# Kernel tuning notes

Measured on AMD Instinct MI355X. Metric: run time of the kernel, lower is better.

The kernel has to match this reference:

```python
import jax, jax.numpy as jnp
import numpy as np

N = 100000      # nodes (single ntype 'paper' for the reference)
R = 4           # relations
E = 300000      # edges per relation
P = 2           # prediction relations (pred_in_n_rev_etypes)
FEAT = 64       # feat_len
H = 64          # gen_h_dim
B = 2           # num_bases
NUM_PRED = 5
S = 4096        # seed nodes


def setup_inputs() -> dict:
    key = jax.random.key(0)
    ks = jax.random.split(key, 26)
    sc = 0.05
    inp = {
        "x": jax.random.normal(ks[0], (N, FEAT), jnp.float32),
        "edges": jax.random.randint(ks[1], (R, E, 2), 0, N, dtype=jnp.int32),
        "seeds": jax.random.randint(ks[2], (S,), 0, N, dtype=jnp.int32),
        "noise": jax.random.normal(ks[3], (N, H), jnp.float32),
        # RelGraphConv layer 1 (basis decomposition) and layer 2
        "V1": jax.random.normal(ks[4], (B, FEAT, H), jnp.float32) * sc,
        "C1": jax.random.normal(ks[5], (R, B), jnp.float32) * sc,
        "V2": jax.random.normal(ks[6], (B, H, H), jnp.float32) * sc,
        "C2": jax.random.normal(ks[7], (R, B), jnp.float32) * sc,
        # per-ntype linear head
        "W_lin": jax.random.normal(ks[8], (H, H), jnp.float32) * sc,
        "b_lin": jnp.zeros((H,), jnp.float32),
        # ReldGen per-relation MLP: H->256->32->1
        "Wd1": jax.random.normal(ks[9], (P, H, 256), jnp.float32) * sc,
        "bd1": jnp.zeros((P, 256), jnp.float32),
        "Wd2": jax.random.normal(ks[10], (P, 256, 32), jnp.float32) * sc,
        "bd2": jnp.zeros((P, 32), jnp.float32),
        "Wd3": jax.random.normal(ks[11], (P, 32, 1), jnp.float32) * sc,
        "bd3": jnp.zeros((P, 1), jnp.float32),
        # RelfGen per-relation MLP: H->256->2048->NUM_PRED*FEAT
        "Wf1": jax.random.normal(ks[12], (P, H, 256), jnp.float32) * sc,
        "bf1": jnp.zeros((P, 256), jnp.float32),
        "Wf2": jax.random.normal(ks[13], (P, 256, 2048), jnp.float32) * sc,
        "bf2": jnp.zeros((P, 2048), jnp.float32),
        "Wf3": jax.random.normal(ks[14], (P, 2048, NUM_PRED * FEAT), jnp.float32) * sc,
        "bf3": jnp.zeros((P, NUM_PRED * FEAT), jnp.float32),
    }
    return inp


def _rel_conv(h, V, C, edges):
    # basis decomposition: W_r = sum_b C[r,b] * V[b]
    Wr = jnp.einsum('rb,bio->rio', C, V)          # [R, in, out]
    m = jnp.einsum('ni,rio->rno', h, Wr)           # transform-then-gather

    def per_rel(m_r, e_r):
        msg = m_r[e_r[:, 0]]                       # gather src  [E, out]
        agg = jax.ops.segment_sum(msg, e_r[:, 1], num_segments=N)
        deg = jax.ops.segment_sum(jnp.ones((e_r.shape[0],), m_r.dtype),
                                  e_r[:, 1], num_segments=N)
        return agg / jnp.maximum(deg, 1.0)[:, None]  # GraphConv norm='right'

    out = jax.vmap(per_rel)(m, edges)              # [R, N, out]
    return jax.nn.relu(out.sum(axis=0))            # HeteroGraphConv 'sum' + relu


def reference(x, edges, seeds, noise, V1, C1, V2, C2, W_lin, b_lin,
              Wd1, bd1, Wd2, bd2, Wd3, bd3, Wf1, bf1, Wf2, bf2, Wf3, bf3):
    h = _rel_conv(x, V1, C1, edges)                # layer 1: FEAT -> H
    h = _rel_conv(h, V2, C2, edges)                # layer 2: H -> H
    h = jax.nn.leaky_relu(h @ W_lin + b_lin)       # per-ntype linear head
    h = h + noise                                  # Sampler: h + N(0,1)
    hs = h[seeds]                                  # [S, H]
    # ReldGen: predicted missing-neighbor counts per relation
    d = jax.nn.leaky_relu(jnp.einsum('sh,phk->psk', hs, Wd1) + bd1[:, None, :])
    d = jax.nn.leaky_relu(jnp.einsum('psk,pkm->psm', d, Wd2) + bd2[:, None, :])
    pred_missing = jax.nn.relu(jnp.einsum('psm,pmo->pso', d, Wd3) + bd3[:, None, :])  # [P,S,1]
    # RelfGen: predicted neighbor features per relation
    f = jax.nn.relu(jnp.einsum('sh,phk->psk', hs, Wf1) + bf1[:, None, :])
    f = jax.nn.relu(jnp.einsum('psk,pkm->psm', f, Wf2) + bf2[:, None, :])
    f = jnp.tanh(jnp.einsum('psm,pmo->pso', f, Wf3) + bf3[:, None, :])
    pred_feat = f.reshape(P, S, NUM_PRED, FEAT)
    return pred_missing, pred_feat
```

## Files before the change

kernel.cpp:

```cpp
#include <hip/hip_runtime.h>
#include <math.h>

#define NN 100000
#define RR 4
#define EE 300000
#define PP 2
#define HH 64
#define SS 4096
#define NSEG (NN * RR)
#define FPART 8
#define PWIDTH ((NN + FPART - 1) / FPART)

typedef __attribute__((ext_vector_type(8))) short short8;
typedef __attribute__((ext_vector_type(4))) short short4v;
typedef __attribute__((ext_vector_type(4))) float f32x4;
typedef __attribute__((ext_vector_type(2))) unsigned int u32x2;

__device__ __forceinline__ short f2bf(float v) {
    unsigned u = __float_as_uint(v);
    unsigned r = (u + 0x7FFFu + ((u >> 16) & 1u)) >> 16;
    return (short)r;
}
__device__ __forceinline__ float bf2f(short s) {
    return __uint_as_float(((unsigned)(unsigned short)s) << 16);
}
__device__ __forceinline__ float bflo(unsigned v) { return __uint_as_float(v << 16); }
__device__ __forceinline__ float bfhi(unsigned v) { return __uint_as_float(v & 0xFFFF0000u); }
__device__ __forceinline__ unsigned pack2(float a, float b) {
    return (unsigned)(unsigned short)f2bf(a) | ((unsigned)(unsigned short)f2bf(b) << 16);
}

struct PrepPtrs {
    const float *Wlin, *Wd1, *Wd2, *Wf1, *Wf2, *Wf3;
    short *Wlin_hi, *Wlin_lo, *Wd1_hi, *Wd1_lo, *Wd2_hi, *Wd2_lo,
          *Wf1_hi, *Wf1_lo, *Wf2_hi, *Wf2_lo, *Wf3_hi, *Wf3_lo;
    const float *C1, *V1, *C2, *V2;
    short *wr1_hi, *wr1_lo, *wr2_hi, *wr2_lo;
    const float *x;
    short *xb;
};

__device__ __forceinline__ void tsp_one(const float* __restrict__ W, short* __restrict__ hi,
                                        short* __restrict__ lo, int K, int N, int idx) {
    int total = K * N;
// ... 131 lines not shown
    if (idx >= RR * EE) return;
    int dst = edges[2 * idx + 1];
    int lo = part * PWIDTH;
    if (dst < lo || dst >= lo + PWIDTH) return;
    int r = idx / EE;
    int src = edges[2 * idx];
    int pos = atomicAdd(&cursor[dst * RR + r], 1);
    csr_src[pos] = src;
}

__global__ __launch_bounds__(256) void gather_agg(const int* __restrict__ row_ptr,
                                                  const int* __restrict__ csr_src,
                                                  const short* __restrict__ feat,
                                                  short* __restrict__ agg) {
    long long tg = (long long)blockIdx.x * 256 + threadIdx.x;
    long long seg = tg >> 4;
    int cl = threadIdx.x & 15;
    if (seg >= (long long)NSEG) return;
    int beg = row_ptr[seg];
    int end = row_ptr[seg + 1];
    float s0 = 0.f, s1 = 0.f, s2 = 0.f, s3 = 0.f;
    int i = beg;
    for (; i + 4 <= end; i += 4) {
        int a = csr_src[i];
        int b = csr_src[i + 1];
        int c = csr_src[i + 2];
        int d = csr_src[i + 3];
        u32x2 va = *(const u32x2*)&feat[a * HH + cl * 4];
        u32x2 vb = *(const u32x2*)&feat[b * HH + cl * 4];
        u32x2 vc = *(const u32x2*)&feat[c * HH + cl * 4];
        u32x2 vd = *(const u32x2*)&feat[d * HH + cl * 4];
        s0 += (bflo(va.x) + bflo(vb.x)) + (bflo(vc.x) + bflo(vd.x));
        s1 += (bfhi(va.x) + bfhi(vb.x)) + (bfhi(vc.x) + bfhi(vd.x));
        s2 += (bflo(va.y) + bflo(vb.y)) + (bflo(vc.y) + bflo(vd.y));
        s3 += (bfhi(va.y) + bfhi(vb.y)) + (bfhi(vc.y) + bfhi(vd.y));
    }
    int rem = end - i;
    if (rem > 0) {
        int a = csr_src[i];
        int b = csr_src[rem > 1 ? i + 1 : i];
        int c = csr_src[rem > 2 ? i + 2 : i];
        u32x2 va = *(const u32x2*)&feat[a * HH + cl * 4];
        u32x2 vb = *(const u32x2*)&feat[b * HH + cl * 4];
        u32x2 vc = *(const u32x2*)&feat[c * HH + cl * 4];
        s0 += bflo(va.x); s1 += bfhi(va.x); s2 += bflo(va.y); s3 += bfhi(va.y);
        if (rem > 1) { s0 += bflo(vb.x); s1 += bfhi(vb.x); s2 += bflo(vb.y); s3 += bfhi(vb.y); }
        if (rem > 2) { s0 += bflo(vc.x); s1 += bfhi(vc.x); s2 += bflo(vc.y); s3 += bfhi(vc.y); }
    }
    int d = end - beg;
    float inv = 1.0f / (float)(d > 1 ? d : 1);
    u32x2 outp;
    outp.x = pack2(s0 * inv, s1 * inv);
    outp.y = pack2(s2 * inv, s3 * inv);
    *(u32x2*)&agg[seg * HH + cl * 4] = outp;
}

__global__ void reduce_tanh(const float* __restrict__ part, const float* __restrict__ bf3,
                            float* __restrict__ out) {
    int idx = blockIdx.x * 256 + threadIdx.x;
    if (idx >= PP * SS * 320) return;
    int p = idx / (SS * 320);
    int rem = idx - p * (SS * 320);
    int n = rem % 320;
    float s = bf3[p * 320 + n];
    #pragma unroll
    for (int ks = 0; ks < 4; ks++)
        s += part[((long long)(p * 4 + ks)) * SS * 320 + rem];
    out[idx] = tanhf(s);
}

template <int ACT, bool OUTBF, int KSPLIT>
__global__ __launch_bounds__(256) void mfma_gemm_bfA(
    const short* __restrict__ A, int lda, long long sA,
    const short* __restrict__ Bhi, const short* __restrict__ Blo, long long sB,
    const float* __restrict__ bias, long long sBias,
    void* __restrict__ Cc, int ldc, long long sC,
    int M, int Nn, int K)
{
    __shared__ short As[128 * 32];
    __shared__ short Bs_hi[64 * 32];
    __shared__ short Bs_lo[64 * 32];

    int z = blockIdx.z;
// ... 69 lines not shown

    #pragma unroll
    for (int s = 0; s < 4; s++) {
        int gmBase = m0 + wm * 64 + s * 16 + quad * 4;
        #pragma unroll
        for (int t = 0; t < 2; t++) {
            int gn = n0 + wn * 32 + t * 16 + mrow;
            if (gn >= Nn) continue;
            float bb = bz ? bz[gn] : 0.f;
            #pragma unroll
            for (int r = 0; r < 4; r++) {
                int gm = gmBase + r;
                if (gm >= M) continue;
                float v = acc[s][t][r] + bb;
                if (ACT == 1) v = fmaxf(v, 0.f);
                else if (ACT == 2) v = (v > 0.f) ? v : 0.01f * v;
                long long co = cbase + (long long)gm * ldc + gn;
                if (OUTBF) ((short*)Cc)[co] = f2bf(v);
                else ((float*)Cc)[co] = v;
            }
        }
    }
}

__global__ __launch_bounds__(256) void combine2_linear(
    const short* __restrict__ A,
    const short* __restrict__ Bhi, const short* __restrict__ Blo,
    const short* __restrict__ Lhi, const short* __restrict__ Llo,
    const float* __restrict__ blin, const float* __restrict__ noise,
    float* __restrict__ h3)
{
    __shared__ short As[128 * 32];
    __shared__ short Bs_hi[64 * 32];
    __shared__ short Bs_lo[64 * 32];
    __shared__ short Ls_hi[64 * 64];
    __shared__ short Ls_lo[64 * 64];
    __shared__ short h2s[128 * 64];

    int tid = threadIdx.x;
    int lane = tid & 63;
    int w = tid >> 6;
    int wm = w >> 1, wn = w & 1;
    int mrow = lane & 15;
    int quad = lane >> 4;
    int m0 = blockIdx.x * 128;

    {
        int base = tid * 16;
        *(short8*)&Ls_hi[base] = *(const short8*)&Lhi[base];
        *(short8*)&Ls_hi[base + 8] = *(const short8*)&Lhi[base + 8];
        *(short8*)&Ls_lo[base] = *(const short8*)&Llo[base];
        *(short8*)&Ls_lo[base + 8] = *(const short8*)&Llo[base + 8];
    }

    f32x4 acc[4][2];
    #pragma unroll
    for (int s = 0; s < 4; s++)
        #pragma unroll
        for (int t = 0; t < 2; t++)
            acc[s][t] = (f32x4){0.f, 0.f, 0.f, 0.f};

    for (int k0 = 0; k0 < 256; k0 += 32) {
        #pragma unroll
        for (int i = 0; i < 2; i++) {
            int f = tid + i * 256;
            int m = f >> 2, q = f & 3;
            int gm = m0 + m;
            short8 av = (short8)0;
            if (gm < NN) av = *(const short8*)&A[(long long)gm * 256 + k0 + q * 8];
            *(short8*)&As[m * 32 + q * 8] = av;
        }
        {
            int n = tid >> 2, q = tid & 3;
            long long boff = (long long)n * 256 + k0 + q * 8;
            *(short8*)&Bs_hi[n * 32 + q * 8] = *(const short8*)&Bhi[boff];
            *(short8*)&Bs_lo[n * 32 + q * 8] = *(const short8*)&Blo[boff];
        }
        __syncthreads();

        short8 ah[4], bh[2], bl[2];
        #pragma unroll
        for (int s = 0; s < 4; s++)
            ah[s] = *(const short8*)&As[(wm * 64 + s * 16 + mrow) * 32 + quad * 8];
        #pragma unroll
        for (int t = 0; t < 2; t++) {
            int soff = (wn * 32 + t * 16 + mrow) * 32 + quad * 8;
            bh[t] = *(const short8*)&Bs_hi[soff];
            bl[t] = *(const short8*)&Bs_lo[soff];
        }
        #pragma unroll
        for (int s = 0; s < 4; s++)
            #pragma unroll
            for (int t = 0; t < 2; t++) {
                acc[s][t] = __builtin_amdgcn_mfma_f32_16x16x32_bf16(ah[s], bh[t], acc[s][t], 0, 0, 0);
                acc[s][t] = __builtin_amdgcn_mfma_f32_16x16x32_bf16(ah[s], bl[t], acc[s][t], 0, 0, 0);
            }
        __syncthreads();
    }

    #pragma unroll
    for (int s = 0; s < 4; s++) {
        int rowB = wm * 64 + s * 16 + quad * 4;
        #pragma unroll
        for (int t = 0; t < 2; t++) {
            int col = wn * 32 + t * 16 + mrow;
            #pragma unroll
            for (int r = 0; r < 4; r++)
                h2s[(rowB + r) * 64 + col] = f2bf(fmaxf(acc[s][t][r], 0.f));
        }
    }
    __syncthreads();

    f32x4 acc2[4][2];
    #pragma unroll
    for (int s = 0; s < 4; s++)
        #pragma unroll
        for (int t = 0; t < 2; t++)
            acc2[s][t] = (f32x4){0.f, 0.f, 0.f, 0.f};

    #pragma unroll
    for (int k0 = 0; k0 < 64; k0 += 32) {
        short8 ah[4], bh[2], bl[2];
        #pragma unroll
        for (int s = 0; s < 4; s++)
            ah[s] = *(const short8*)&h2s[(wm * 64 + s * 16 + mrow) * 64 + k0 + quad * 8];
        #pragma unroll
        for (int t = 0; t < 2; t++) {
            int soff = (wn * 32 + t * 16 + mrow) * 64 + k0 + quad * 8;
            bh[t] = *(const short8*)&Ls_hi[soff];
            bl[t] = *(const short8*)&Ls_lo[soff];
        }
        #pragma unroll
        for (int s = 0; s < 4; s++)
            #pragma unroll
            for (int t = 0; t < 2; t++) {
                acc2[s][t] = __builtin_amdgcn_mfma_f32_16x16x32_bf16(ah[s], bh[t], acc2[s][t], 0, 0, 0);
                acc2[s][t] = __builtin_amdgcn_mfma_f32_16x16x32_bf16(ah[s], bl[t], acc2[s][t], 0, 0, 0);
            }
    }

    #pragma unroll
    for (int s = 0; s < 4; s++) {
        int gmBase = m0 + wm * 64 + s * 16 + quad * 4;
        #pragma unroll
        for (int t = 0; t < 2; t++) {
            int gn = wn * 32 + t * 16 + mrow;
            float bb = blin[gn];
            #pragma unroll
            for (int r = 0; r < 4; r++) {
                int gm = gmBase + r;
                if (gm >= NN) continue;
                float v = acc2[s][t][r] + bb;
                v = (v > 0.f) ? v : 0.01f * v;
                v += noise[(long long)gm * 64 + gn];
                h3[(long long)gm * 64 + gn] = v;
            }
        }
    }
}

__global__ __launch_bounds__(256) void head1_gemm(
    const float* __restrict__ h3, const int* __restrict__ seeds,
    const short* __restrict__ Bd_hi, const short* __restrict__ Bd_lo, const float* __restrict__ bd,
    const short* __restrict__ Bf_hi, const short* __restrict__ Bf_lo, const float* __restrict__ bfb,
    short* __restrict__ outd, short* __restrict__ outf)
{
    __shared__ short As_hi[128 * 32];
    __shared__ short As_lo[128 * 32];
    __shared__ short Bs_hi[64 * 32];
    __shared__ short Bs_lo[64 * 32];

    int z = blockIdx.z;
    int head = z >> 1, p = z & 1;
    const short* Bhi = (head ? Bf_hi : Bd_hi) + (long long)p * 256 * 64;
    const short* Blo = (head ? Bf_lo : Bd_lo) + (long long)p * 256 * 64;
    const float* bz = (head ? bfb : bd) + p * 256;
    short* Cc = (head ? outf : outd) + (long long)p * SS * 256;

    int m0 = blockIdx.y * 128;
    int n0 = blockIdx.x * 64;
    int tid = threadIdx.x;
    int lane = tid & 63;
    int w = tid >> 6;
    int wm = w >> 1, wn = w & 1;
    int mrow = lane & 15;
    int quad = lane >> 4;

    f32x4 acc[4][2];
    #pragma unroll
    for (int s = 0; s < 4; s++)
        #pragma unroll
        for (int t = 0; t < 2; t++)
            acc[s][t] = (f32x4){0.f, 0.f, 0.f, 0.f};

    #pragma unroll
    for (int k0 = 0; k0 < 64; k0 += 32) {
        #pragma unroll
        for (int i = 0; i < 4; i++) {
            int f = tid + i * 256;
            int m = f >> 3, k4 = f & 7;
            int node = seeds[m0 + m];
            f32x4 v = *(const f32x4*)&h3[(long long)node * 64 + k0 + k4 * 4];
            short4v hv, lv;
            #pragma unroll
            for (int c = 0; c < 4; c++) {
                short hh = f2bf(v[c]);
                hv[c] = hh;
                lv[c] = f2bf(v[c] - bf2f(hh));
            }
            *(short4v*)&As_hi[m * 32 + k4 * 4] = hv;
            *(short4v*)&As_lo[m * 32 + k4 * 4] = lv;
        }
        {
            int n = tid >> 2, q = tid & 3;
            long long boff = (long long)(n0 + n) * 64 + k0 + q * 8;
            *(short8*)&Bs_hi[n * 32 + q * 8] = *(const short8*)&Bhi[boff];
            *(short8*)&Bs_lo[n * 32 + q * 8] = *(const short8*)&Blo[boff];
        }
        __syncthreads();

        short8 ah[4], al[4], bh[2], bl[2];
        #pragma unroll
        for (int s = 0; s < 4; s++) {
            int soff = (wm * 64 + s * 16 + mrow) * 32 + quad * 8;
            ah[s] = *(const short8*)&As_hi[soff];
            al[s] = *(const short8*)&As_lo[soff];
        }
        #pragma unroll
        for (int t = 0; t < 2; t++) {
            int soff = (wn * 32 + t * 16 + mrow) * 32 + quad * 8;
            bh[t] = *(const short8*)&Bs_hi[soff];
            bl[t] = *(const short8*)&Bs_lo[soff];
        }
        #pragma unroll
        for (int s = 0; s < 4; s++)
            #pragma unroll
            for (int t = 0; t < 2; t++) {
                acc[s][t] = __builtin_amdgcn_mfma_f32_16x16x32_bf16(ah[s], bh[t], acc[s][t], 0, 0, 0);
                acc[s][t] = __builtin_amdgcn_mfma_f32_16x16x32_bf16(ah[s], bl[t], acc[s][t], 0, 0, 0);
                acc[s][t] = __builtin_amdgcn_mfma_f32_16x16x32_bf16(al[s], bh[t], acc[s][t], 0, 0, 0);
            }
        __syncthreads();
    }

    #pragma unroll
    for (int s = 0; s < 4; s++) {
        int gmBase = m0 + wm * 64 + s * 16 + quad * 4;
        #pragma unroll
        for (int t = 0; t < 2; t++) {
            int gn = n0 + wn * 32 + t * 16 + mrow;
            float bb = bz[gn];
            #pragma unroll
            for (int r = 0; r < 4; r++) {
                int gm = gmBase + r;
                float v = acc[s][t][r] + bb;
                v = (head == 1) ? fmaxf(v, 0.f) : ((v > 0.f) ? v : 0.01f * v);
                Cc[(long long)gm * 256 + gn] = f2bf(v);
            }
        }
    }
}

__global__ __launch_bounds__(256) void dhead_gemm(
    const short* __restrict__ d1b,
    const short* __restrict__ Bhi, const short* __restrict__ Blo,
    const float* __restrict__ bd2, const float* __restrict__ Wd3,
    const float* __restrict__ bd3, float* __restrict__ out)
{
    __shared__ short As[128 * 32];
    __shared__ short Bs_hi[64 * 32];
    __shared__ short Bs_lo[64 * 32];
    __shared__ float d2s[128][33];

    int p = blockIdx.z;
    const short* A = d1b + (long long)p * SS * 256;
    const short* Bh = Bhi + (long long)p * 32 * 256;
    const short* Bl = Blo + (long long)p * 32 * 256;

    int m0 = blockIdx.y * 128;
    int tid = threadIdx.x;
    int lane = tid & 63;
    int w = tid >> 6;
    int wm = w >> 1, wn = w & 1;
    int mrow = lane & 15;
    int quad = lane >> 4;

    f32x4 acc[4][2];
    #pragma unroll
    for (int s = 0; s < 4; s++)
        #pragma unroll
        for (int t = 0; t < 2; t++)
            acc[s][t] = (f32x4){0.f, 0.f, 0.f, 0.f};

    for (int k0 = 0; k0 < 256; k0 += 32) {
        #pragma unroll
        for (int i = 0; i < 2; i++) {
            int f = tid + i * 256;
            int m = f >> 2, q = f & 3;
            *(short8*)&As[m * 32 + q * 8] = *(const short8*)&A[(long long)(m0 + m) * 256 + k0 + q * 8];
        }
        {
            int n = tid >> 2, q = tid & 3;
            short8 bh = (short8)0, bl = (short8)0;
            if (n < 32) {
                long long boff = (long long)n * 256 + k0 + q * 8;
                bh = *(const short8*)&Bh[boff];
                bl = *(const short8*)&Bl[boff];
            }
            *(short8*)&Bs_hi[n * 32 + q * 8] = bh;
            *(short8*)&Bs_lo[n * 32 + q * 8] = bl;
        }
        __syncthreads();

        short8 ah[4], bh[2], bl[2];
        #pragma unroll
        for (int s = 0; s < 4; s++)
            ah[s] = *(const short8*)&As[(wm * 64 + s * 16 + mrow) * 32 + quad * 8];
        #pragma unroll
        for (int t = 0; t < 2; t++) {
            int soff = (wn * 32 + t * 16 + mrow) * 32 + quad * 8;
            bh[t] = *(const short8*)&Bs_hi[soff];
            bl[t] = *(const short8*)&Bs_lo[soff];
        }
        #pragma unroll
        for (int s = 0; s < 4; s++)
            #pragma unroll
            for (int t = 0; t < 2; t++) {
                acc[s][t] = __builtin_amdgcn_mfma_f32_16x16x32_bf16(ah[s], bh[t], acc[s][t], 0, 0, 0);
                acc[s][t] = __builtin_amdgcn_mfma_f32_16x16x32_bf16(ah[s], bl[t], acc[s][t], 0, 0, 0);
            }
        __syncthreads();
    }

    if (wn == 0) {
        #pragma unroll
        for (int s = 0; s < 4; s++) {
            int rowB = wm * 64 + s * 16 + quad * 4;
            #pragma unroll
            for (int t = 0; t < 2; t++) {
                int col = t * 16 + mrow;
                #pragma unroll
                for (int r = 0; r < 4; r++) {
                    float v = acc[s][t][r] + bd2[p * 32 + col];
                    d2s[rowB + r][col] = (v > 0.f) ? v : 0.01f * v;
                }
            }
        }
    }
    __syncthreads();

    if (tid < 128) {
        float sacc = bd3[p];
        #pragma unroll
        for (int k = 0; k < 32; k++) sacc += d2s[tid][k] * Wd3[p * 32 + k];
        out[p * SS + m0 + tid] = fmaxf(sacc, 0.f);
    }
}

extern "C" void kernel_launch(void* const* d_in, const int* in_sizes, int n_in,
                              void* d_out, int out_size, void* d_ws, size_t ws_size,
                              hipStream_t stream) {
    const float* x    = (const float*)d_in[0];
    const int* edges  = (const int*)d_in[1];
    const int* seeds  = (const int*)d_in[2];
    const float* noise= (const float*)d_in[3];
    const float* V1   = (const float*)d_in[4];
    const float* C1   = (const float*)d_in[5];
    const float* V2   = (const float*)d_in[6];
    const float* C2   = (const float*)d_in[7];
    const float* Wlin = (const float*)d_in[8];
    const float* blin = (const float*)d_in[9];
    const float* Wd1 = (const float*)d_in[10]; const float* bd1 = (const float*)d_in[11];
    const float* Wd2 = (const float*)d_in[12]; const float* bd2 = (const float*)d_in[13];
    const float* Wd3 = (const float*)d_in[14]; const float* bd3 = (const float*)d_in[15];
    const float* Wf1 = (const float*)d_in[16]; const float* bf1 = (const float*)d_in[17];
    const float* Wf2 = (const float*)d_in[18]; const float* bf2 = (const float*)d_in[19];
    const float* Wf3 = (const float*)d_in[20]; const float* bf3 = (const float*)d_in[21];

    float* out = (float*)d_out;

    char* ws = (char*)d_ws;
    size_t off = 0;
    auto allocf = [&](size_t nf) {
        float* p = (float*)(ws + off);
        off += ((nf * 4 + 255) / 256) * 256;
        return p;
    };
    auto allocs = [&](size_t ns) {
        short* p = (short*)(ws + off);
        off += ((ns * 2 + 255) / 256) * 256;
        return p;
    };
    auto alloci = [&](size_t ni) {
        int* p = (int*)(ws + off);
        off += ((ni * 4 + 255) / 256) * 256;
        return p;
    };

    short* Wrt1_hi = allocs(16384);          short* Wrt1_lo = allocs(16384);
    short* Wrt2_hi = allocs(16384);          short* Wrt2_lo = allocs(16384);
    short* Wlint_hi = allocs(4096);          short* Wlint_lo = allocs(4096);
    short* Wd1t_hi = allocs(2 * 64 * 256);   short* Wd1t_lo = allocs(2 * 64 * 256);
    short* Wd2t_hi = allocs(2 * 256 * 32);   short* Wd2t_lo = allocs(2 * 256 * 32);
    short* Wf1t_hi = allocs(2 * 64 * 256);   short* Wf1t_lo = allocs(2 * 64 * 256);
    short* Wf2t_hi = allocs((size_t)2 * 256 * 2048);  short* Wf2t_lo = allocs((size_t)2 * 256 * 2048);
    short* Wf3t_hi = allocs((size_t)2 * 2048 * 320);  short* Wf3t_lo = allocs((size_t)2 * 2048 * 320);

    int* counts  = alloci(NSEG);
    int* excl    = alloci(NSEG);
    int* bsums   = alloci(2048);
    int* row_ptr = alloci(NSEG + 1);
    int* cursor  = alloci(NSEG);
    int* csr_src = alloci((size_t)RR * EE);

    short* xb  = allocs((size_t)NN * HH);
    short* agg = allocs((size_t)NSEG * HH);
    short* h1  = allocs((size_t)NN * HH);
    float* h3  = allocf((size_t)NN * HH);
    short* d1b = allocs((size_t)PP * SS * 256);
    short* f1  = allocs((size_t)PP * SS * 256);
    short* f2b = allocs((size_t)PP * SS * 2048);

    float* fpart = (float*)agg;

    PrepPtrs pp;
    pp.Wlin = Wlin; pp.Wd1 = Wd1; pp.Wd2 = Wd2; pp.Wf1 = Wf1; pp.Wf2 = Wf2; pp.Wf3 = Wf3;
    pp.Wlin_hi = Wlint_hi; pp.Wlin_lo = Wlint_lo;
    pp.Wd1_hi = Wd1t_hi;   pp.Wd1_lo = Wd1t_lo;
    pp.Wd2_hi = Wd2t_hi;   pp.Wd2_lo = Wd2t_lo;
    pp.Wf1_hi = Wf1t_hi;   pp.Wf1_lo = Wf1t_lo;
    pp.Wf2_hi = Wf2t_hi;   pp.Wf2_lo = Wf2t_lo;
    pp.Wf3_hi = Wf3t_hi;   pp.Wf3_lo = Wf3t_lo;
    pp.C1 = C1; pp.V1 = V1; pp.C2 = C2; pp.V2 = V2;
    pp.wr1_hi = Wrt1_hi; pp.wr1_lo = Wrt1_lo; pp.wr2_hi = Wrt2_hi; pp.wr2_lo = Wrt2_lo;
    pp.x = x; pp.xb = xb;
    prep_all<<<WR_BLK + TSP_BLK + XB_BLK, 256, 0, stream>>>(pp);

    hipMemsetAsync(counts, 0, (size_t)NSEG * 4, stream);
    int eb0 = (RR * EE + 255) / 256;
    count_kernel<<<eb0, 256, 0, stream>>>(edges, counts);
    int nb = (NSEG + 255) / 256;
    scan1<<<nb, 256, 0, stream>>>(counts, excl, bsums, NSEG);
    scan2<<<1, 256, 0, stream>>>(bsums, nb);
    scan3<<<nb, 256, 0, stream>>>(excl, bsums, row_ptr, cursor, NSEG, RR * EE);
    fill_csr<<<eb0 * FPART, 256, 0, stream>>>(edges, cursor, csr_src);

    int gb = (int)(((long long)NSEG * 16 + 255) / 256);
    int MY = (NN + 127) / 128;

    gather_agg<<<gb, 256, 0, stream>>>(row_ptr, csr_src, xb, agg);
    mfma_gemm_bfA<1, true, 1><<<dim3(1, MY, 1), 256, 0, stream>>>(
        agg, 256, 0, Wrt1_hi, Wrt1_lo, 0, nullptr, 0,
        h1, 64, 0, NN, 64, 256);

    gather_agg<<<gb, 256, 0, stream>>>(row_ptr, csr_src, h1, agg);
    combine2_linear<<<MY, 256, 0, stream>>>(
        agg, Wrt2_hi, Wrt2_lo, Wlint_hi, Wlint_lo, blin, noise, h3);

    head1_gemm<<<dim3(4, 32, 4), 256, 0, stream>>>(
        h3, seeds, Wd1t_hi, Wd1t_lo, bd1, Wf1t_hi, Wf1t_lo, bf1, d1b, f1);

    dhead_gemm<<<dim3(1, 32, PP), 256, 0, stream>>>(
        d1b, Wd2t_hi, Wd2t_lo, bd2, Wd3, bd3, out);

    mfma_gemm_bfA<1, true, 1><<<dim3(32, 32, PP), 256, 0, stream>>>(
        f1, 256, (long long)SS * 256, Wf2t_hi, Wf2t_lo, (long long)2048 * 256, bf2, 2048,
        f2b, 2048, (long long)SS * 2048, SS, 2048, 256);
    mfma_gemm_bfA<0, false, 4><<<dim3(5, 32, PP * 4), 256, 0, stream>>>(
        f2b, 2048, (long long)SS * 2048, Wf3t_hi, Wf3t_lo, (long long)320 * 2048, nullptr, 0,
        fpart, 320, (long long)SS * 320, SS, 320, 2048);
    reduce_tanh<<<(PP * SS * 320 + 255) / 256, 256, 0, stream>>>(fpart, bf3, out + (size_t)PP * SS);
}
```

Measured before the change: 529.1 us.

## Widen gather loads, shrink combine tiles, store h3 as bf16

The gather kernel now gives each thread 8 bf16 columns through 16-byte loads, using half as many threads per segment. The layer-1 and layer-2 combine kernels move to 64-row tiles; combine2 reuses one shared buffer for the h2 tile and keeps the linear weights in registers, which cuts LDS use so more blocks can be resident. h3 is stored as bf16 rather than fp32, so head1 loads seed rows directly and drops the split hi/lo A operand, saving one MFMA per tile step. The trade is lower precision in the h3 path.

```diff
diff --git a/kernel.cpp b/kernel.cpp
--- a/kernel.cpp
+++ b/kernel.cpp
@@ -14,7 +14,6 @@
 typedef __attribute__((ext_vector_type(8))) short short8;
 typedef __attribute__((ext_vector_type(4))) short short4v;
 typedef __attribute__((ext_vector_type(4))) float f32x4;
-typedef __attribute__((ext_vector_type(2))) unsigned int u32x2;
 
 __device__ __forceinline__ short f2bf(float v) {
     unsigned u = __float_as_uint(v);
@@ -23,11 +22,6 @@
 }
 __device__ __forceinline__ float bf2f(short s) {
     return __uint_as_float(((unsigned)(unsigned short)s) << 16);
-}
-__device__ __forceinline__ float bflo(unsigned v) { return __uint_as_float(v << 16); }
-__device__ __forceinline__ float bfhi(unsigned v) { return __uint_as_float(v & 0xFFFF0000u); }
-__device__ __forceinline__ unsigned pack2(float a, float b) {
-    return (unsigned)(unsigned short)f2bf(a) | ((unsigned)(unsigned short)f2bf(b) << 16);
 }
 
 struct PrepPtrs {
@@ -189,45 +183,47 @@
                                                   const short* __restrict__ feat,
                                                   short* __restrict__ agg) {
     long long tg = (long long)blockIdx.x * 256 + threadIdx.x;
-    long long seg = tg >> 4;
-    int cl = threadIdx.x & 15;
+    long long seg = tg >> 3;
+    int cl = threadIdx.x & 7;
     if (seg >= (long long)NSEG) return;
     int beg = row_ptr[seg];
     int end = row_ptr[seg + 1];
-    float s0 = 0.f, s1 = 0.f, s2 = 0.f, s3 = 0.f;
+    float s[8] = {0.f, 0.f, 0.f, 0.f, 0.f, 0.f, 0.f, 0.f};
     int i = beg;
     for (; i + 4 <= end; i += 4) {
         int a = csr_src[i];
         int b = csr_src[i + 1];
         int c = csr_src[i + 2];
         int d = csr_src[i + 3];
-        u32x2 va = *(const u32x2*)&feat[a * HH + cl * 4];
-        u32x2 vb = *(const u32x2*)&feat[b * HH + cl * 4];
-        u32x2 vc = *(const u32x2*)&feat[c * HH + cl * 4];
-        u32x2 vd = *(const u32x2*)&feat[d * HH + cl * 4];
-        s0 += (bflo(va.x) + bflo(vb.x)) + (bflo(vc.x) + bflo(vd.x));
-        s1 += (bfhi(va.x) + bfhi(vb.x)) + (bfhi(vc.x) + bfhi(vd.x));
-        s2 += (bflo(va.y) + bflo(vb.y)) + (bflo(vc.y) + bflo(vd.y));
-        s3 += (bfhi(va.y) + bfhi(vb.y)) + (bfhi(vc.y) + bfhi(vd.y));
+        short8 va = *(const short8*)&feat[a * HH + cl * 8];
+        short8 vb = *(const short8*)&feat[b * HH + cl * 8];
+        short8 vc = *(const short8*)&feat[c * HH + cl * 8];
+        short8 vd = *(const short8*)&feat[d * HH + cl * 8];
+        #pragma unroll
+        for (int j = 0; j < 8; j++)
+            s[j] += (bf2f(va[j]) + bf2f(vb[j])) + (bf2f(vc[j]) + bf2f(vd[j]));
     }
     int rem = end - i;
     if (rem > 0) {
         int a = csr_src[i];
         int b = csr_src[rem > 1 ? i + 1 : i];
         int c = csr_src[rem > 2 ? i + 2 : i];
-        u32x2 va = *(const u32x2*)&feat[a * HH + cl * 4];
-        u32x2 vb = *(const u32x2*)&feat[b * HH + cl * 4];
-        u32x2 vc = *(const u32x2*)&feat[c * HH + cl * 4];
-        s0 += bflo(va.x); s1 += bfhi(va.x); s2 += bflo(va.y); s3 += bfhi(va.y);
-        if (rem > 1) { s0 += bflo(vb.x); s1 += bfhi(vb.x); s2 += bflo(vb.y); s3 += bfhi(vb.y); }
-        if (rem > 2) { s0 += bflo(vc.x); s1 += bfhi(vc.x); s2 += bflo(vc.y); s3 += bfhi(vc.y); }
+        short8 va = *(const short8*)&feat[a * HH + cl * 8];
+        short8 vb = *(const short8*)&feat[b * HH + cl * 8];
+        short8 vc = *(const short8*)&feat[c * HH + cl * 8];
+        #pragma unroll
+        for (int j = 0; j < 8; j++) {
+            s[j] += bf2f(va[j]);
+            s[j] += (rem > 1) ? bf2f(vb[j]) : 0.f;
+            s[j] += (rem > 2) ? bf2f(vc[j]) : 0.f;
+        }
     }
     int d = end - beg;
     float inv = 1.0f / (float)(d > 1 ? d : 1);
-    u32x2 outp;
-    outp.x = pack2(s0 * inv, s1 * inv);
-    outp.y = pack2(s2 * inv, s3 * inv);
-    *(u32x2*)&agg[seg * HH + cl * 4] = outp;
+    short8 o;
+    #pragma unroll
+    for (int j = 0; j < 8; j++) o[j] = f2bf(s[j] * inv);
+    *(short8*)&agg[seg * HH + cl * 8] = o;
 }
 
 __global__ void reduce_tanh(const float* __restrict__ part, const float* __restrict__ bf3,
@@ -242,6 +238,385 @@
     for (int ks = 0; ks < 4; ks++)
         s += part[((long long)(p * 4 + ks)) * SS * 320 + rem];
     out[idx] = tanhf(s);
+}
+
+__global__ __launch_bounds__(256) void combine1_kernel(
+    const short* __restrict__ A,
+    const short* __restrict__ Bhi, const short* __restrict__ Blo,
+    short* __restrict__ h1)
+{
+    __shared__ short As[64 * 32];
+    __shared__ short Bs_hi[64 * 32];
+    __shared__ short Bs_lo[64 * 32];
+
+    int tid = threadIdx.x;
+    int lane = tid & 63;
+    int w = tid >> 6, wm = w >> 1, wn = w & 1;
+    int mrow = lane & 15, quad = lane >> 4;
+    int m0 = blockIdx.x * 64;
+
+    f32x4 acc[2][2];
+    #pragma unroll
+    for (int s = 0; s < 2; s++)
+        #pragma unroll
+        for (int t = 0; t < 2; t++)
+            acc[s][t] = (f32x4){0.f, 0.f, 0.f, 0.f};
+
+    for (int k0 = 0; k0 < 256; k0 += 32) {
+        {
+            int m = tid >> 2, q = tid & 3;
+            int gm = m0 + m;
+            short8 av = (short8)0;
+            if (gm < NN) av = *(const short8*)&A[(long long)gm * 256 + k0 + q * 8];
+            *(short8*)&As[m * 32 + q * 8] = av;
+            long long boff = (long long)m * 256 + k0 + q * 8;
+            *(short8*)&Bs_hi[m * 32 + q * 8] = *(const short8*)&Bhi[boff];
+            *(short8*)&Bs_lo[m * 32 + q * 8] = *(const short8*)&Blo[boff];
+        }
+        __syncthreads();
+
+        short8 ah[2], bh[2], bl[2];
+        #pragma unroll
+        for (int s = 0; s < 2; s++)
+            ah[s] = *(const short8*)&As[(wm * 32 + s * 16 + mrow) * 32 + quad * 8];
+        #pragma unroll
+        for (int t = 0; t < 2; t++) {
+            int soff = (wn * 32 + t * 16 + mrow) * 32 + quad * 8;
+            bh[t] = *(const short8*)&Bs_hi[soff];
+            bl[t] = *(const short8*)&Bs_lo[soff];
+        }
+        #pragma unroll
+        for (int s = 0; s < 2; s++)
+            #pragma unroll
+            for (int t = 0; t < 2; t++) {
+                acc[s][t] = __builtin_amdgcn_mfma_f32_16x16x32_bf16(ah[s], bh[t], acc[s][t], 0, 0, 0);
+                acc[s][t] = __builtin_amdgcn_mfma_f32_16x16x32_bf16(ah[s], bl[t], acc[s][t], 0, 0, 0);
+            }
+        __syncthreads();
+    }
+
+    #pragma unroll
+    for (int s = 0; s < 2; s++) {
+        int gmBase = m0 + wm * 32 + s * 16 + quad * 4;
+        #pragma unroll
+        for (int t = 0; t < 2; t++) {
+            int gn = wn * 32 + t * 16 + mrow;
+            #pragma unroll
+            for (int r = 0; r < 4; r++) {
+                int gm = gmBase + r;
+                if (gm >= NN) continue;
+                h1[(long long)gm * 64 + gn] = f2bf(fmaxf(acc[s][t][r], 0.f));
+            }
+        }
+    }
+}
+
+__global__ __launch_bounds__(256) void combine2_linear(
+    const short* __restrict__ A,
+    const short* __restrict__ Bhi, const short* __restrict__ Blo,
+    const short* __restrict__ Lhi, const short* __restrict__ Llo,
+    const float* __restrict__ blin, const float* __restrict__ noise,
+    short* __restrict__ h3b)
+{
+    __shared__ short smem[6144];
+    short* As = smem;
+    short* Bs_hi = smem + 2048;
+    short* Bs_lo = smem + 4096;
+    short* h2s = smem;
+
+    int tid = threadIdx.x;
+    int lane = tid & 63;
+    int w = tid >> 6, wm = w >> 1, wn = w & 1;
+    int mrow = lane & 15, quad = lane >> 4;
+    int m0 = blockIdx.x * 64;
+
+    short8 lhi[2][2], llo[2][2];
+    #pragma unroll
+    for (int t = 0; t < 2; t++)
+        #pragma unroll
+        for (int kk = 0; kk < 2; kk++) {
+            int loff = (wn * 32 + t * 16 + mrow) * 64 + kk * 32 + quad * 8;
+            lhi[t][kk] = *(const short8*)&Lhi[loff];
+            llo[t][kk] = *(const short8*)&Llo[loff];
+        }
+
+    f32x4 acc[2][2];
+    #pragma unroll
+    for (int s = 0; s < 2; s++)
+        #pragma unroll
+        for (int t = 0; t < 2; t++)
+            acc[s][t] = (f32x4){0.f, 0.f, 0.f, 0.f};
+
+    for (int k0 = 0; k0 < 256; k0 += 32) {
+        {
+            int m = tid >> 2, q = tid & 3;
+            int gm = m0 + m;
+            short8 av = (short8)0;
+            if (gm < NN) av = *(const short8*)&A[(long long)gm * 256 + k0 + q * 8];
+            *(short8*)&As[m * 32 + q * 8] = av;
+            long long boff = (long long)m * 256 + k0 + q * 8;
+            *(short8*)&Bs_hi[m * 32 + q * 8] = *(const short8*)&Bhi[boff];
+            *(short8*)&Bs_lo[m * 32 + q * 8] = *(const short8*)&Blo[boff];
+        }
+        __syncthreads();
+
+        short8 ah[2], bh[2], bl[2];
+        #pragma unroll
+        for (int s = 0; s < 2; s++)
+            ah[s] = *(const short8*)&As[(wm * 32 + s * 16 + mrow) * 32 + quad * 8];
+        #pragma unroll
+        for (int t = 0; t < 2; t++) {
+            int soff = (wn * 32 + t * 16 + mrow) * 32 + quad * 8;
+            bh[t] = *(const short8*)&Bs_hi[soff];
+            bl[t] = *(const short8*)&Bs_lo[soff];
+        }
+        #pragma unroll
+        for (int s = 0; s < 2; s++)
+            #pragma unroll
+            for (int t = 0; t < 2; t++) {
+                acc[s][t] = __builtin_amdgcn_mfma_f32_16x16x32_bf16(ah[s], bh[t], acc[s][t], 0, 0, 0);
+                acc[s][t] = __builtin_amdgcn_mfma_f32_16x16x32_bf16(ah[s], bl[t], acc[s][t], 0, 0, 0);
+            }
+        __syncthreads();
+    }
+
+    #pragma unroll
+    for (int s = 0; s < 2; s++) {
+        int rowB = wm * 32 + s * 16 + quad * 4;
+        #pragma unroll
+        for (int t = 0; t < 2; t++) {
+            int col = wn * 32 + t * 16 + mrow;
+            #pragma unroll
+            for (int r = 0; r < 4; r++)
+                h2s[(rowB + r) * 72 + col] = f2bf(fmaxf(acc[s][t][r], 0.f));
+        }
+    }
+    __syncthreads();
+
+    f32x4 acc2[2][2];
+    #pragma unroll
+    for (int s = 0; s < 2; s++)
+        #pragma unroll
+        for (int t = 0; t < 2; t++)
+            acc2[s][t] = (f32x4){0.f, 0.f, 0.f, 0.f};
+
+    #pragma unroll
+    for (int kk = 0; kk < 2; kk++) {
+        short8 ah[2];
+        #pragma unroll
+        for (int s = 0; s < 2; s++)
+            ah[s] = *(const short8*)&h2s[(wm * 32 + s * 16 + mrow) * 72 + kk * 32 + quad * 8];
+        #pragma unroll
+        for (int s = 0; s < 2; s++)
+            #pragma unroll
+            for (int t = 0; t < 2; t++) {
+                acc2[s][t] = __builtin_amdgcn_mfma_f32_16x16x32_bf16(ah[s], lhi[t][kk], acc2[s][t], 0, 0, 0);
+                acc2[s][t] = __builtin_amdgcn_mfma_f32_16x16x32_bf16(ah[s], llo[t][kk], acc2[s][t], 0, 0, 0);
+            }
+    }
+
+    #pragma unroll
+    for (int s = 0; s < 2; s++) {
+        int gmBase = m0 + wm * 32 + s * 16 + quad * 4;
+        #pragma unroll
+        for (int t = 0; t < 2; t++) {
+            int gn = wn * 32 + t * 16 + mrow;
+            float bb = blin[gn];
+            #pragma unroll
+            for (int r = 0; r < 4; r++) {
+                int gm = gmBase + r;
+                if (gm >= NN) continue;
+                float v = acc2[s][t][r] + bb;
+                v = (v > 0.f) ? v : 0.01f * v;
+                v += noise[(long long)gm * 64 + gn];
+                h3b[(long long)gm * 64 + gn] = f2bf(v);
+            }
+        }
+    }
+}
+
+__global__ __launch_bounds__(256) void head1_gemm(
+    const short* __restrict__ h3b, const int* __restrict__ seeds,
+    const short* __restrict__ Bd_hi, const short* __restrict__ Bd_lo, const float* __restrict__ bd,
+    const short* __restrict__ Bf_hi, const short* __restrict__ Bf_lo, const float* __restrict__ bfb,
+    short* __restrict__ outd, short* __restrict__ outf)
+{
+    __shared__ short As[128 * 32];
+    __shared__ short Bs_hi[64 * 32];
+    __shared__ short Bs_lo[64 * 32];
+
+    int z = blockIdx.z;
+    int head = z >> 1, p = z & 1;
+    const short* Bhi = (head ? Bf_hi : Bd_hi) + (long long)p * 256 * 64;
+    const short* Blo = (head ? Bf_lo : Bd_lo) + (long long)p * 256 * 64;
+    const float* bz = (head ? bfb : bd) + p * 256;
+    short* Cc = (head ? outf : outd) + (long long)p * SS * 256;
+
+    int m0 = blockIdx.y * 128;
+    int n0 = blockIdx.x * 64;
+    int tid = threadIdx.x;
+    int lane = tid & 63;
+    int w = tid >> 6;
+    int wm = w >> 1, wn = w & 1;
+    int mrow = lane & 15;
+    int quad = lane >> 4;
+
+    f32x4 acc[4][2];
+    #pragma unroll
+    for (int s = 0; s < 4; s++)
+        #pragma unroll
+        for (int t = 0; t < 2; t++)
+            acc[s][t] = (f32x4){0.f, 0.f, 0.f, 0.f};
+
+    #pragma unroll
+    for (int k0 = 0; k0 < 64; k0 += 32) {
+        #pragma unroll
+        for (int i = 0; i < 2; i++) {
+            int f = tid + i * 256;
+            int m = f >> 2, q = f & 3;
+            int node = seeds[m0 + m];
+            *(short8*)&As[m * 32 + q * 8] = *(const short8*)&h3b[(long long)node * 64 + k0 + q * 8];
+        }
+        {
+            int n = tid >> 2, q = tid & 3;
+            long long boff = (long long)(n0 + n) * 64 + k0 + q * 8;
+            *(short8*)&Bs_hi[n * 32 + q * 8] = *(const short8*)&Bhi[boff];
+            *(short8*)&Bs_lo[n * 32 + q * 8] = *(const short8*)&Blo[boff];
+        }
+        __syncthreads();
+
+        short8 ah[4], bh[2], bl[2];
+        #pragma unroll
+        for (int s = 0; s < 4; s++)
+            ah[s] = *(const short8*)&As[(wm * 64 + s * 16 + mrow) * 32 + quad * 8];
+        #pragma unroll
+        for (int t = 0; t < 2; t++) {
+            int soff = (wn * 32 + t * 16 + mrow) * 32 + quad * 8;
+            bh[t] = *(const short8*)&Bs_hi[soff];
+            bl[t] = *(const short8*)&Bs_lo[soff];
+        }
+        #pragma unroll
+        for (int s = 0; s < 4; s++)
+            #pragma unroll
+            for (int t = 0; t < 2; t++) {
+                acc[s][t] = __builtin_amdgcn_mfma_f32_16x16x32_bf16(ah[s], bh[t], acc[s][t], 0, 0, 0);
+                acc[s][t] = __builtin_amdgcn_mfma_f32_16x16x32_bf16(ah[s], bl[t], acc[s][t], 0, 0, 0);
+            }
+        __syncthreads();
+    }
+
+    #pragma unroll
+    for (int s = 0; s < 4; s++) {
+        int gmBase = m0 + wm * 64 + s * 16 + quad * 4;
+        #pragma unroll
+        for (int t = 0; t < 2; t++) {
+            int gn = n0 + wn * 32 + t * 16 + mrow;
+            float bb = bz[gn];
+            #pragma unroll
+            for (int r = 0; r < 4; r++) {
+                int gm = gmBase + r;
+                float v = acc[s][t][r] + bb;
+                v = (head == 1) ? fmaxf(v, 0.f) : ((v > 0.f) ? v : 0.01f * v);
+                Cc[(long long)gm * 256 + gn] = f2bf(v);
+            }
+        }
+    }
+}
+
+__global__ __launch_bounds__(256) void dhead_gemm(
+    const short* __restrict__ d1b,
+    const short* __restrict__ Bhi, const short* __restrict__ Blo,
+    const float* __restrict__ bd2, const float* __restrict__ Wd3,
+    const float* __restrict__ bd3, float* __restrict__ out)
+{
+    __shared__ short As[128 * 32];
+    __shared__ short Bs_hi[64 * 32];
+    __shared__ short Bs_lo[64 * 32];
+    __shared__ float d2s[128][33];
+
+    int p = blockIdx.z;
+    const short* A = d1b + (long long)p * SS * 256;
+    const short* Bh = Bhi + (long long)p * 32 * 256;
+    const short* Bl = Blo + (long long)p * 32 * 256;
+
+    int m0 = blockIdx.y * 128;
+    int tid = threadIdx.x;
+    int lane = tid & 63;
+    int w = tid >> 6;
+    int wm = w >> 1, wn = w & 1;
+    int mrow = lane & 15;
+    int quad = lane >> 4;
+
+    f32x4 acc[4][2];
+    #pragma unroll
+    for (int s = 0; s < 4; s++)
+        #pragma unroll
+        for (int t = 0; t < 2; t++)
+            acc[s][t] = (f32x4){0.f, 0.f, 0.f, 0.f};
+
+    for (int k0 = 0; k0 < 256; k0 += 32) {
+        #pragma unroll
+        for (int i = 0; i < 2; i++) {
+            int f = tid + i * 256;
+            int m = f >> 2, q = f & 3;
+            *(short8*)&As[m * 32 + q * 8] = *(const short8*)&A[(long long)(m0 + m) * 256 + k0 + q * 8];
+        }
+        {
+            int n = tid >> 2, q = tid & 3;
+            short8 bh = (short8)0, bl = (short8)0;
+            if (n < 32) {
+                long long boff = (long long)n * 256 + k0 + q * 8;
+                bh = *(const short8*)&Bh[boff];
+                bl = *(const short8*)&Bl[boff];
+            }
+            *(short8*)&Bs_hi[n * 32 + q * 8] = bh;
+            *(short8*)&Bs_lo[n * 32 + q * 8] = bl;
+        }
+        __syncthreads();
+
+        short8 ah[4], bh[2], bl[2];
+        #pragma unroll
+        for (int s = 0; s < 4; s++)
+            ah[s] = *(const short8*)&As[(wm * 64 + s * 16 + mrow) * 32 + quad * 8];
+        #pragma unroll
+        for (int t = 0; t < 2; t++) {
+            int soff = (wn * 32 + t * 16 + mrow) * 32 + quad * 8;
+            bh[t] = *(const short8*)&Bs_hi[soff];
+            bl[t] = *(const short8*)&Bs_lo[soff];
+        }
+        #pragma unroll
+        for (int s = 0; s < 4; s++)
+            #pragma unroll
+            for (int t = 0; t < 2; t++) {
+                acc[s][t] = __builtin_amdgcn_mfma_f32_16x16x32_bf16(ah[s], bh[t], acc[s][t], 0, 0, 0);
+                acc[s][t] = __builtin_amdgcn_mfma_f32_16x16x32_bf16(ah[s], bl[t], acc[s][t], 0, 0, 0);
+            }
+        __syncthreads();
+    }
+
+    if (wn == 0) {
+        #pragma unroll
+        for (int s = 0; s < 4; s++) {
+            int rowB = wm * 64 + s * 16 + quad * 4;
+            #pragma unroll
+            for (int t = 0; t < 2; t++) {
+                int col = t * 16 + mrow;
+                #pragma unroll
+                for (int r = 0; r < 4; r++) {
+                    float v = acc[s][t][r] + bd2[p * 32 + col];
+                    d2s[rowB + r][col] = (v > 0.f) ? v : 0.01f * v;
+                }
+            }
+        }
+    }
+    __syncthreads();
+
+    if (tid < 128) {
+        float sacc = bd3[p];
+        #pragma unroll
+        for (int k = 0; k < 32; k++) sacc += d2s[tid][k] * Wd3[p * 32 + k];
+        out[p * SS + m0 + tid] = fmaxf(sacc, 0.f);
+    }
 }
 
 template <int ACT, bool OUTBF, int KSPLIT>
@@ -341,346 +716,11 @@
                 if (gm >= M) continue;
                 float v = acc[s][t][r] + bb;
                 if (ACT == 1) v = fmaxf(v, 0.f);
-                else if (ACT == 2) v = (v > 0.f) ? v : 0.01f * v;
                 long long co = cbase + (long long)gm * ldc + gn;
                 if (OUTBF) ((short*)Cc)[co] = f2bf(v);
                 else ((float*)Cc)[co] = v;
             }
         }
-    }
-}
-
-__global__ __launch_bounds__(256) void combine2_linear(
-    const short* __restrict__ A,
-    const short* __restrict__ Bhi, const short* __restrict__ Blo,
-    const short* __restrict__ Lhi, const short* __restrict__ Llo,
-    const float* __restrict__ blin, const float* __restrict__ noise,
-    float* __restrict__ h3)
-{
-    __shared__ short As[128 * 32];
-    __shared__ short Bs_hi[64 * 32];
-    __shared__ short Bs_lo[64 * 32];
-    __shared__ short Ls_hi[64 * 64];
-    __shared__ short Ls_lo[64 * 64];
-    __shared__ short h2s[128 * 64];
-
-    int tid = threadIdx.x;
-    int lane = tid & 63;
-    int w = tid >> 6;
-    int wm = w >> 1, wn = w & 1;
-    int mrow = lane & 15;
-    int quad = lane >> 4;
-    int m0 = blockIdx.x * 128;
-
-    {
-        int base = tid * 16;
-        *(short8*)&Ls_hi[base] = *(const short8*)&Lhi[base];
-        *(short8*)&Ls_hi[base + 8] = *(const short8*)&Lhi[base + 8];
-        *(short8*)&Ls_lo[base] = *(const short8*)&Llo[base];
-        *(short8*)&Ls_lo[base + 8] = *(const short8*)&Llo[base + 8];
-    }
-
-    f32x4 acc[4][2];
-    #pragma unroll
-    for (int s = 0; s < 4; s++)
-        #pragma unroll
-        for (int t = 0; t < 2; t++)
-            acc[s][t] = (f32x4){0.f, 0.f, 0.f, 0.f};
-
-    for (int k0 = 0; k0 < 256; k0 += 32) {
-        #pragma unroll
-        for (int i = 0; i < 2; i++) {
-            int f = tid + i * 256;
-            int m = f >> 2, q = f & 3;
-            int gm = m0 + m;
-            short8 av = (short8)0;
-            if (gm < NN) av = *(const short8*)&A[(long long)gm * 256 + k0 + q * 8];
-            *(short8*)&As[m * 32 + q * 8] = av;
-        }
-        {
-            int n = tid >> 2, q = tid & 3;
-            long long boff = (long long)n * 256 + k0 + q * 8;
-            *(short8*)&Bs_hi[n * 32 + q * 8] = *(const short8*)&Bhi[boff];
-            *(short8*)&Bs_lo[n * 32 + q * 8] = *(const short8*)&Blo[boff];
-        }
-        __syncthreads();
-
-        short8 ah[4], bh[2], bl[2];
-        #pragma unroll
-        for (int s = 0; s < 4; s++)
-            ah[s] = *(const short8*)&As[(wm * 64 + s * 16 + mrow) * 32 + quad * 8];
-        #pragma unroll
-        for (int t = 0; t < 2; t++) {
-            int soff = (wn * 32 + t * 16 + mrow) * 32 + quad * 8;
-            bh[t] = *(const short8*)&Bs_hi[soff];
-            bl[t] = *(const short8*)&Bs_lo[soff];
-        }
-        #pragma unroll
-        for (int s = 0; s < 4; s++)
-            #pragma unroll
-            for (int t = 0; t < 2; t++) {
-                acc[s][t] = __builtin_amdgcn_mfma_f32_16x16x32_bf16(ah[s], bh[t], acc[s][t], 0, 0, 0);
-                acc[s][t] = __builtin_amdgcn_mfma_f32_16x16x32_bf16(ah[s], bl[t], acc[s][t], 0, 0, 0);
-            }
-        __syncthreads();
-    }
-
-    #pragma unroll
-    for (int s = 0; s < 4; s++) {
-        int rowB = wm * 64 + s * 16 + quad * 4;
-        #pragma unroll
-        for (int t = 0; t < 2; t++) {
-            int col = wn * 32 + t * 16 + mrow;
-            #pragma unroll
-            for (int r = 0; r < 4; r++)
-                h2s[(rowB + r) * 64 + col] = f2bf(fmaxf(acc[s][t][r], 0.f));
-        }
-    }
-    __syncthreads();
-
-    f32x4 acc2[4][2];
-    #pragma unroll
-    for (int s = 0; s < 4; s++)
-        #pragma unroll
-        for (int t = 0; t < 2; t++)
-            acc2[s][t] = (f32x4){0.f, 0.f, 0.f, 0.f};
-
-    #pragma unroll
-    for (int k0 = 0; k0 < 64; k0 += 32) {
-        short8 ah[4], bh[2], bl[2];
-        #pragma unroll
-        for (int s = 0; s < 4; s++)
-            ah[s] = *(const short8*)&h2s[(wm * 64 + s * 16 + mrow) * 64 + k0 + quad * 8];
-        #pragma unroll
-        for (int t = 0; t < 2; t++) {
-            int soff = (wn * 32 + t * 16 + mrow) * 64 + k0 + quad * 8;
-            bh[t] = *(const short8*)&Ls_hi[soff];
-            bl[t] = *(const short8*)&Ls_lo[soff];
-        }
-        #pragma unroll
-        for (int s = 0; s < 4; s++)
-            #pragma unroll
-            for (int t = 0; t < 2; t++) {
-                acc2[s][t] = __builtin_amdgcn_mfma_f32_16x16x32_bf16(ah[s], bh[t], acc2[s][t], 0, 0, 0);
-                acc2[s][t] = __builtin_amdgcn_mfma_f32_16x16x32_bf16(ah[s], bl[t], acc2[s][t], 0, 0, 0);
-            }
-    }
-
-    #pragma unroll
-    for (int s = 0; s < 4; s++) {
-        int gmBase = m0 + wm * 64 + s * 16 + quad * 4;
-        #pragma unroll
-        for (int t = 0; t < 2; t++) {
-            int gn = wn * 32 + t * 16 + mrow;
-            float bb = blin[gn];
-            #pragma unroll
-            for (int r = 0; r < 4; r++) {
-                int gm = gmBase + r;
-                if (gm >= NN) continue;
-                float v = acc2[s][t][r] + bb;
-                v = (v > 0.f) ? v : 0.01f * v;
-                v += noise[(long long)gm * 64 + gn];
-                h3[(long long)gm * 64 + gn] = v;
-            }
-        }
-    }
-}
-
-__global__ __launch_bounds__(256) void head1_gemm(
-    const float* __restrict__ h3, const int* __restrict__ seeds,
-    const short* __restrict__ Bd_hi, const short* __restrict__ Bd_lo, const float* __restrict__ bd,
-    const short* __restrict__ Bf_hi, const short* __restrict__ Bf_lo, const float* __restrict__ bfb,
-    short* __restrict__ outd, short* __restrict__ outf)
-{
-    __shared__ short As_hi[128 * 32];
-    __shared__ short As_lo[128 * 32];
-    __shared__ short Bs_hi[64 * 32];
-    __shared__ short Bs_lo[64 * 32];
-
-    int z = blockIdx.z;
-    int head = z >> 1, p = z & 1;
-    const short* Bhi = (head ? Bf_hi : Bd_hi) + (long long)p * 256 * 64;
-    const short* Blo = (head ? Bf_lo : Bd_lo) + (long long)p * 256 * 64;
-    const float* bz = (head ? bfb : bd) + p * 256;
-    short* Cc = (head ? outf : outd) + (long long)p * SS * 256;
-
-    int m0 = blockIdx.y * 128;
-    int n0 = blockIdx.x * 64;
-    int tid = threadIdx.x;
-    int lane = tid & 63;
-    int w = tid >> 6;
-    int wm = w >> 1, wn = w & 1;
-    int mrow = lane & 15;
-    int quad = lane >> 4;
-
-    f32x4 acc[4][2];
-    #pragma unroll
-    for (int s = 0; s < 4; s++)
-        #pragma unroll
-        for (int t = 0; t < 2; t++)
-            acc[s][t] = (f32x4){0.f, 0.f, 0.f, 0.f};
-
-    #pragma unroll
-    for (int k0 = 0; k0 < 64; k0 += 32) {
-        #pragma unroll
-        for (int i = 0; i < 4; i++) {
-            int f = tid + i * 256;
-            int m = f >> 3, k4 = f & 7;
-            int node = seeds[m0 + m];
-            f32x4 v = *(const f32x4*)&h3[(long long)node * 64 + k0 + k4 * 4];
-            short4v hv, lv;
-            #pragma unroll
-            for (int c = 0; c < 4; c++) {
-                short hh = f2bf(v[c]);
-                hv[c] = hh;
-                lv[c] = f2bf(v[c] - bf2f(hh));
-            }
-            *(short4v*)&As_hi[m * 32 + k4 * 4] = hv;
-            *(short4v*)&As_lo[m * 32 + k4 * 4] = lv;
-        }
-        {
-            int n = tid >> 2, q = tid & 3;
-            long long boff = (long long)(n0 + n) * 64 + k0 + q * 8;
-            *(short8*)&Bs_hi[n * 32 + q * 8] = *(const short8*)&Bhi[boff];
-            *(short8*)&Bs_lo[n * 32 + q * 8] = *(const short8*)&Blo[boff];
-        }
-        __syncthreads();
-
-        short8 ah[4], al[4], bh[2], bl[2];
-        #pragma unroll
-        for (int s = 0; s < 4; s++) {
-            int soff = (wm * 64 + s * 16 + mrow) * 32 + quad * 8;
-            ah[s] = *(const short8*)&As_hi[soff];
-            al[s] = *(const short8*)&As_lo[soff];
-        }
-        #pragma unroll
-        for (int t = 0; t < 2; t++) {
-            int soff = (wn * 32 + t * 16 + mrow) * 32 + quad * 8;
-            bh[t] = *(const short8*)&Bs_hi[soff];
-            bl[t] = *(const short8*)&Bs_lo[soff];
-        }
-        #pragma unroll
-        for (int s = 0; s < 4; s++)
-            #pragma unroll
-            for (int t = 0; t < 2; t++) {
-                acc[s][t] = __builtin_amdgcn_mfma_f32_16x16x32_bf16(ah[s], bh[t], acc[s][t], 0, 0, 0);
-                acc[s][t] = __builtin_amdgcn_mfma_f32_16x16x32_bf16(ah[s], bl[t], acc[s][t], 0, 0, 0);
-                acc[s][t] = __builtin_amdgcn_mfma_f32_16x16x32_bf16(al[s], bh[t], acc[s][t], 0, 0, 0);
-            }
-        __syncthreads();
-    }
-
-    #pragma unroll
-    for (int s = 0; s < 4; s++) {
-        int gmBase = m0 + wm * 64 + s * 16 + quad * 4;
-        #pragma unroll
-        for (int t = 0; t < 2; t++) {
-            int gn = n0 + wn * 32 + t * 16 + mrow;
-            float bb = bz[gn];
-            #pragma unroll
-            for (int r = 0; r < 4; r++) {
-                int gm = gmBase + r;
-                float v = acc[s][t][r] + bb;
-                v = (head == 1) ? fmaxf(v, 0.f) : ((v > 0.f) ? v : 0.01f * v);
-                Cc[(long long)gm * 256 + gn] = f2bf(v);
-            }
-        }
-    }
-}
-
-__global__ __launch_bounds__(256) void dhead_gemm(
-    const short* __restrict__ d1b,
-    const short* __restrict__ Bhi, const short* __restrict__ Blo,
-    const float* __restrict__ bd2, const float* __restrict__ Wd3,
-    const float* __restrict__ bd3, float* __restrict__ out)
-{
-    __shared__ short As[128 * 32];
-    __shared__ short Bs_hi[64 * 32];
-    __shared__ short Bs_lo[64 * 32];
-    __shared__ float d2s[128][33];
-
-    int p = blockIdx.z;
-    const short* A = d1b + (long long)p * SS * 256;
-    const short* Bh = Bhi + (long long)p * 32 * 256;
-    const short* Bl = Blo + (long long)p * 32 * 256;
-
-    int m0 = blockIdx.y * 128;
-    int tid = threadIdx.x;
-    int lane = tid & 63;
-    int w = tid >> 6;
-    int wm = w >> 1, wn = w & 1;
-    int mrow = lane & 15;
-    int quad = lane >> 4;
-
-    f32x4 acc[4][2];
-    #pragma unroll
-    for (int s = 0; s < 4; s++)
-        #pragma unroll
-        for (int t = 0; t < 2; t++)
-            acc[s][t] = (f32x4){0.f, 0.f, 0.f, 0.f};
-
-    for (int k0 = 0; k0 < 256; k0 += 32) {
-        #pragma unroll
-        for (int i = 0; i < 2; i++) {
-            int f = tid + i * 256;
-            int m = f >> 2, q = f & 3;
-            *(short8*)&As[m * 32 + q * 8] = *(const short8*)&A[(long long)(m0 + m) * 256 + k0 + q * 8];
-        }
-        {
-            int n = tid >> 2, q = tid & 3;
-            short8 bh = (short8)0, bl = (short8)0;
-            if (n < 32) {
-                long long boff = (long long)n * 256 + k0 + q * 8;
-                bh = *(const short8*)&Bh[boff];
-                bl = *(const short8*)&Bl[boff];
-            }
-            *(short8*)&Bs_hi[n * 32 + q * 8] = bh;
-            *(short8*)&Bs_lo[n * 32 + q * 8] = bl;
-        }
-        __syncthreads();
-
-        short8 ah[4], bh[2], bl[2];
-        #pragma unroll
-        for (int s = 0; s < 4; s++)
-            ah[s] = *(const short8*)&As[(wm * 64 + s * 16 + mrow) * 32 + quad * 8];
-        #pragma unroll
-        for (int t = 0; t < 2; t++) {
-            int soff = (wn * 32 + t * 16 + mrow) * 32 + quad * 8;
-            bh[t] = *(const short8*)&Bs_hi[soff];
-            bl[t] = *(const short8*)&Bs_lo[soff];
-        }
-        #pragma unroll
-        for (int s = 0; s < 4; s++)
-            #pragma unroll
-            for (int t = 0; t < 2; t++) {
-                acc[s][t] = __builtin_amdgcn_mfma_f32_16x16x32_bf16(ah[s], bh[t], acc[s][t], 0, 0, 0);
-                acc[s][t] = __builtin_amdgcn_mfma_f32_16x16x32_bf16(ah[s], bl[t], acc[s][t], 0, 0, 0);
-            }
-        __syncthreads();
-    }
-
-    if (wn == 0) {
-        #pragma unroll
-        for (int s = 0; s < 4; s++) {
-            int rowB = wm * 64 + s * 16 + quad * 4;
-            #pragma unroll
-            for (int t = 0; t < 2; t++) {
-                int col = t * 16 + mrow;
-                #pragma unroll
-                for (int r = 0; r < 4; r++) {
-                    float v = acc[s][t][r] + bd2[p * 32 + col];
-                    d2s[rowB + r][col] = (v > 0.f) ? v : 0.01f * v;
-                }
-            }
-        }
-    }
-    __syncthreads();
-
-    if (tid < 128) {
-        float sacc = bd3[p];
-        #pragma unroll
-        for (int k = 0; k < 32; k++) sacc += d2s[tid][k] * Wd3[p * 32 + k];
-        out[p * SS + m0 + tid] = fmaxf(sacc, 0.f);
     }
 }
 
@@ -708,11 +748,6 @@
 
     char* ws = (char*)d_ws;
     size_t off = 0;
-    auto allocf = [&](size_t nf) {
-        float* p = (float*)(ws + off);
-        off += ((nf * 4 + 255) / 256) * 256;
-        return p;
-    };
     auto allocs = [&](size_t ns) {
         short* p = (short*)(ws + off);
         off += ((ns * 2 + 255) / 256) * 256;
@@ -743,7 +778,7 @@
     short* xb  = allocs((size_t)NN * HH);
     short* agg = allocs((size_t)NSEG * HH);
     short* h1  = allocs((size_t)NN * HH);
-    float* h3  = allocf((size_t)NN * HH);
+    short* h3b = allocs((size_t)NN * HH);
     short* d1b = allocs((size_t)PP * SS * 256);
     short* f1  = allocs((size_t)PP * SS * 256);
     short* f2b = allocs((size_t)PP * SS * 2048);
@@ -772,20 +807,18 @@
     scan3<<<nb, 256, 0, stream>>>(excl, bsums, row_ptr, cursor, NSEG, RR * EE);
     fill_csr<<<eb0 * FPART, 256, 0, stream>>>(edges, cursor, csr_src);
 
-    int gb = (int)(((long long)NSEG * 16 + 255) / 256);
-    int MY = (NN + 127) / 128;
+    int gb = (int)(((long long)NSEG * 8 + 255) / 256);
+    int MB64 = (NN + 63) / 64;
 
     gather_agg<<<gb, 256, 0, stream>>>(row_ptr, csr_src, xb, agg);
-    mfma_gemm_bfA<1, true, 1><<<dim3(1, MY, 1), 256, 0, stream>>>(
-        agg, 256, 0, Wrt1_hi, Wrt1_lo, 0, nullptr, 0,
-        h1, 64, 0, NN, 64, 256);
+    combine1_kernel<<<MB64, 256, 0, stream>>>(agg, Wrt1_hi, Wrt1_lo, h1);
 
     gather_agg<<<gb, 256, 0, stream>>>(row_ptr, csr_src, h1, agg);
-    combine2_linear<<<MY, 256, 0, stream>>>(
-        agg, Wrt2_hi, Wrt2_lo, Wlint_hi, Wlint_lo, blin, noise, h3);
+    combine2_linear<<<MB64, 256, 0, stream>>>(
+        agg, Wrt2_hi, Wrt2_lo, Wlint_hi, Wlint_lo, blin, noise, h3b);
 
     head1_gemm<<<dim3(4, 32, 4), 256, 0, stream>>>(
-        h3, seeds, Wd1t_hi, Wd1t_lo, bd1, Wf1t_hi, Wf1t_lo, bf1, d1b, f1);
+        h3b, seeds, Wd1t_hi, Wd1t_lo, bd1, Wf1t_hi, Wf1t_lo, bf1, d1b, f1);
 
     dhead_gemm<<<dim3(1, 32, PP), 256, 0, stream>>>(
         d1b, Wd2t_hi, Wd2t_lo, bd2, Wd3, bd3, out);
```

After: 481.6 us. 1.1x faster.
